# Kernel optimization log

Hardware: AMD Instinct MI355X
Metric: run time of the kernel (lower is better)

## Reference

```python
import jax, jax.numpy as jnp
import numpy as np

SHIFTS = 1
WINDOW_SIZES = (4, 8, 16)
BN_EPS = 1e-5


def _calc_attn_path(x, ws, shifts):
    # x: (b, H, W, 2c) with channels laid out as (qv=2, c)
    b, H, W, c2 = x.shape
    c = c2 // 2
    if shifts > 0:
        x = jnp.roll(x, shift=(-ws // 2, -ws // 2), axis=(1, 2))
    h, w = H // ws, W // ws
    # 'b (h dh) (w dw) (qv c) -> qv (b h w) (dh dw c)'
    qv = x.reshape(b, h, ws, w, ws, 2, c).transpose(5, 0, 1, 3, 2, 4, 6)
    qv = qv.reshape(2, b * h * w, ws * ws * c)
    q, v = qv[0], qv[1]                       # (N, D), N = b*h*w windows, D = ws*ws*c
    atn = jax.nn.softmax(q @ q.T, axis=-1)    # (N, N) attention across windows (as in source)
    y = atn @ v                               # (N, D)
    # '(b h w) (dh dw c) -> b (h dh) (w dw) c'
    y = y.reshape(b, h, w, ws, ws, c).transpose(0, 1, 3, 2, 4, 5).reshape(b, H, W, c)
    if shifts > 0:
        y = jnp.roll(y, shift=(ws // 2, ws // 2), axis=(1, 2))
    return y, atn


def setup_inputs() -> dict:
    key = jax.random.key(0)
    ks = jax.random.split(key, 3)
    B, H, W, C = 4, 128, 128, 180
    inputs = jax.random.normal(ks[0], (B, H, W, C), jnp.float32)
    conv1_w = jax.random.normal(ks[1], (1, 1, C, 2 * C), jnp.float32) * 0.05
    conv1_b = jnp.zeros((2 * C,), jnp.float32)
    bn_scale = jnp.ones((2 * C,), jnp.float32)
    bn_bias = jnp.zeros((2 * C,), jnp.float32)
    conv2_w = jax.random.normal(ks[2], (1, 1, C, C), jnp.float32) * 0.05
    conv2_b = jnp.zeros((C,), jnp.float32)
    return {"inputs": inputs, "conv1_w": conv1_w, "conv1_b": conv1_b,
            "bn_scale": bn_scale, "bn_bias": bn_bias,
            "conv2_w": conv2_w, "conv2_b": conv2_b}


def reference(inputs, conv1_w, conv1_b, bn_scale, bn_bias, conv2_w, conv2_b):
    # 1x1 conv to 2*C channels (calc_attn=True)
    x = jnp.einsum('bhwc,cd->bhwd', inputs, conv1_w[0, 0]) + conv1_b
    # BatchNorm in training mode (batch statistics)
    mean = x.mean(axis=(0, 1, 2))
    var = x.var(axis=(0, 1, 2))
    x = (x - mean) * jax.lax.rsqrt(var + BN_EPS) * bn_scale + bn_bias
    xs = jnp.split(x, 3, axis=-1)             # three groups of 2*C/3 channels
    ys, attns = [], []
    for ws, xi in zip(WINDOW_SIZES, xs):
        y, a = _calc_attn_path(xi, ws, SHIFTS)
        ys.append(y)
        attns.append(a)
    y = jnp.concatenate(ys, axis=-1)          # back to C channels
    y = jnp.einsum('bhwc,cd->bhwd', y, conv2_w[0, 0]) + conv2_b
    return (y, *attns)
```

## Files before the change

kernel.cpp:

```cpp
#include <hip/hip_runtime.h>

typedef unsigned short u16;
typedef __bf16 bf16x8 __attribute__((ext_vector_type(8)));
typedef float f32x4 __attribute__((ext_vector_type(4)));
typedef u16 u16x4 __attribute__((ext_vector_type(4)));
typedef u16 u16x8 __attribute__((ext_vector_type(8)));

__device__ __forceinline__ u16 f2bf(float v) {
    unsigned u = __float_as_uint(v);
    unsigned r = (u + 0x7fffu + ((u >> 16) & 1u)) >> 16;
    return (u16)r;
}
__device__ __forceinline__ float bf2f(u16 u) { return __uint_as_float(((unsigned)u) << 16); }

__device__ __forceinline__ void async_cp16(const u16* g, u16* l) {
    __builtin_amdgcn_global_load_lds((const __attribute__((address_space(1))) unsigned int*)g,
                                     (__attribute__((address_space(3))) unsigned int*)l, 16, 0, 0);
}

__device__ __forceinline__ int xcd_swz(int local, int n) {
    const int q = n >> 3, r = n & 7;
    const int xcd = local & 7, j = local >> 3;
    const int base = xcd < r ? xcd * (q + 1) : r * (q + 1) + (xcd - r) * q;
    return base + j;
}

#define LKSWZ(tid) ((((tid) & 3) ^ (((tid) >> 3) & 3)) << 3)
#define ROSWZ(lane) (((lane) & 15) * 32 + ((((lane) >> 4) ^ (((lane) >> 1) & 3)) << 3))

__global__ __launch_bounds__(256) void gemm_f32(
    const u16* __restrict__ A, const u16* __restrict__ B,
    float* __restrict__ C, const float* __restrict__ bias,
    int K, int ldc, int n_store)
{
    __shared__ char smem[32768];
    u16* As = (u16*)smem;
    u16* Bs = (u16*)(smem + 8192);
    const int tid = threadIdx.x;
    const int lane = tid & 63;
    const int wave = tid >> 6;
    const int wm = wave >> 1, wn = wave & 1;
    const long m0 = (long)blockIdx.y * 128;
    const long n0 = (long)blockIdx.x * 128;

    f32x4 acc[4][4] = {};
    const int lrow = tid >> 2;
    const int lk = LKSWZ(tid);
    const u16* Ag = A + (m0 + lrow) * (long)K + lk;
    const u16* Bg = B + (n0 + lrow) * (long)K + lk;
    u16* Asl = As + tid * 8;
    u16* Bsl = Bs + tid * 8;
    const long K64 = (long)64 * K;
    const int ro = ROSWZ(lane);
    const int nsteps = K >> 5;

    async_cp16(Ag, Asl);
    async_cp16(Ag + K64, Asl + 2048);
    async_cp16(Bg, Bsl);
    async_cp16(Bg + K64, Bsl + 2048);
    __syncthreads();

    int cur = 0;
    for (int s = 0; s < nsteps; s++) {
        if (s + 1 < nsteps) {
            const int kn = (s + 1) << 5;
            u16* An = Asl + ((cur ^ 1) << 13);
            u16* Bn = Bsl + ((cur ^ 1) << 13);
            async_cp16(Ag + kn, An);
            async_cp16(Ag + kn + K64, An + 2048);
            async_cp16(Bg + kn, Bn);
            async_cp16(Bg + kn + K64, Bn + 2048);
        }
        bf16x8 af[4], bg[4];
        const u16* Asc = As + (cur << 13);
        const u16* Bsc = Bs + (cur << 13);
#pragma unroll
        for (int i = 0; i < 4; i++) af[i] = *(const bf16x8*)(Asc + (wm * 64 + i * 16) * 32 + ro);
#pragma unroll
        for (int j = 0; j < 4; j++) bg[j] = *(const bf16x8*)(Bsc + (wn * 64 + j * 16) * 32 + ro);
#pragma unroll
        for (int i = 0; i < 4; i++)
#pragma unroll
            for (int j = 0; j < 4; j++)
                acc[i][j] = __builtin_amdgcn_mfma_f32_16x16x32_bf16(af[i], bg[j], acc[i][j], 0, 0, 0);
        __syncthreads();
        cur ^= 1;
    }

    float bv[4];
#pragma unroll
    for (int j = 0; j < 4; j++) bv[j] = bias[n0 + wn * 64 + j * 16 + (lane & 15)];

    float* Cs = (float*)smem;
    for (int c = 0; c < 4; c++) {
        __syncthreads();
        if (wm == (c >> 1)) {
#pragma unroll
            for (int ii = 0; ii < 2; ii++) {
                const int i = (c & 1) * 2 + ii;
#pragma unroll
                for (int j = 0; j < 4; j++)
#pragma unroll
                    for (int r = 0; r < 4; r++) {
                        const int lr = ii * 16 + ((lane >> 4) << 2) + r;
                        Cs[lr * 128 + wn * 64 + j * 16 + (lane & 15)] = acc[i][j][r] + bv[j];
                    }
            }
        }
        __syncthreads();
        const int lr = tid >> 3;
        const int cg = (tid & 7) * 16;
        const long rowg = m0 + c * 32 + lr;
#pragma unroll
        for (int e = 0; e < 4; e++) {
            const int colg = cg + e * 4;
            if ((int)n0 + colg < n_store)
                *(f32x4*)(C + rowg * (long)ldc + n0 + colg) = *(const f32x4*)(Cs + lr * 128 + colg);
        }
    }
}

__global__ __launch_bounds__(256) void conv1_gemm(
    const float* __restrict__ A, const u16* __restrict__ B,
    u16* __restrict__ C, const float* __restrict__ bias)
{
    __shared__ char smem[16384];
    u16* As = (u16*)smem;
    u16* Bs = (u16*)(smem + 8192);
    const int tid = threadIdx.x;
    const int lane = tid & 63;
    const int wave = tid >> 6;
    const int wm = wave >> 1, wn = wave & 1;
    const long m0 = (long)blockIdx.y * 128;
    const long n0 = (long)blockIdx.x * 128;

    f32x4 acc[4][4] = {};
    const int lrow = tid >> 2;
    const int lk = LKSWZ(tid);
    const float* Ar0 = A + (m0 + lrow) * 180L;
    const float* Ar1 = Ar0 + 64 * 180L;
    const u16* Bg = B + (n0 + lrow) * 192L + lk;
    u16* Asl = As + tid * 8;
    u16* Bsl = Bs + tid * 8;
    const int ro = ROSWZ(lane);

#pragma unroll
    for (int k0 = 0; k0 < 192; k0 += 32) {
        const int gk = k0 + lk;
        u16x8 oa, ob;
        if (gk + 8 <= 180) {
            f32x4 a0 = *(const f32x4*)(Ar0 + gk), a1 = *(const f32x4*)(Ar0 + gk + 4);
            f32x4 b0 = *(const f32x4*)(Ar1 + gk), b1 = *(const f32x4*)(Ar1 + gk + 4);
#pragma unroll
            for (int c = 0; c < 4; c++) {
                oa[c] = f2bf(a0[c]); oa[4 + c] = f2bf(a1[c]);
                ob[c] = f2bf(b0[c]); ob[4 + c] = f2bf(b1[c]);
            }
        } else if (gk < 180) {
            f32x4 a0 = *(const f32x4*)(Ar0 + gk);
            f32x4 b0 = *(const f32x4*)(Ar1 + gk);
#pragma unroll
            for (int c = 0; c < 4; c++) {
                oa[c] = f2bf(a0[c]); oa[4 + c] = 0;
                ob[c] = f2bf(b0[c]); ob[4 + c] = 0;
            }
        } else {
#pragma unroll
            for (int c = 0; c < 8; c++) { oa[c] = 0; ob[c] = 0; }
        }
        *(u16x8*)Asl = oa;
        *(u16x8*)(Asl + 2048) = ob;
        async_cp16(Bg + k0, Bsl);
        async_cp16(Bg + k0 + 64 * 192, Bsl + 2048);
        __syncthreads();
        bf16x8 af[4], bg[4];
#pragma unroll
        for (int i = 0; i < 4; i++) af[i] = *(const bf16x8*)(As + (wm * 64 + i * 16) * 32 + ro);
#pragma unroll
        for (int j = 0; j < 4; j++) bg[j] = *(const bf16x8*)(Bs + (wn * 64 + j * 16) * 32 + ro);
#pragma unroll
        for (int i = 0; i < 4; i++)
#pragma unroll
            for (int j = 0; j < 4; j++)
                acc[i][j] = __builtin_amdgcn_mfma_f32_16x16x32_bf16(af[i], bg[j], acc[i][j], 0, 0, 0);
        __syncthreads();
    }

    float bv[4];
#pragma unroll
    for (int j = 0; j < 4; j++) bv[j] = bias[n0 + wn * 64 + j * 16 + (lane & 15)];

    u16* Cs = (u16*)smem;
    for (int c = 0; c < 2; c++) {
        __syncthreads();
        if (wm == c) {
#pragma unroll
            for (int i = 0; i < 4; i++)
#pragma unroll
                for (int j = 0; j < 4; j++)
#pragma unroll
                    for (int r = 0; r < 4; r++) {
                        const int lr = i * 16 + ((lane >> 4) << 2) + r;
                        Cs[lr * 128 + wn * 64 + j * 16 + (lane & 15)] = f2bf(acc[i][j][r] + bv[j]);
                    }
        }
        __syncthreads();
        const int lr = tid >> 2;
        const int cg = (tid & 3) * 32;
        const long rowg = m0 + c * 64 + lr;
#pragma unroll
        for (int e = 0; e < 4; e++) {
            const int colg = cg + e * 8;
            *(u16x8*)(C + rowg * 384L + n0 + colg) = *(const u16x8*)(Cs + lr * 128 + colg);
        }
    }
}

__global__ __launch_bounds__(256) void qq_all(
    const u16* __restrict__ q0, const u16* __restrict__ q1, const u16* __restrict__ q2,
    float* __restrict__ S0, float* __restrict__ pG1, float* __restrict__ pG2)
{
    __shared__ char smem[32768];
    u16* As = (u16*)smem;
    u16* Bs = (u16*)(smem + 8192);
    const int bid = blockIdx.x;
    int seg, local;
    if (bid < 528) { seg = 0; local = xcd_swz(bid, 528); }
    else if (bid < 816) { seg = 1; local = xcd_swz(bid - 528, 288); }
    else { seg = 2; local = xcd_swz(bid - 816, 180); }
    const int tX = seg == 0 ? 32 : (seg == 1 ? 8 : 2);
    const int TT = (tX * (tX + 1)) >> 1;
    const int K = seg == 0 ? 1024 : (seg == 1 ? 3840 : 15360);
    const int Ksplit = seg == 0 ? 1024 : (seg == 1 ? 480 : 256);
    const int N = seg == 0 ? 4096 : (seg == 1 ? 1024 : 256);
    const u16* A = seg == 0 ? q0 : (seg == 1 ? q1 : q2);
    float* outP = seg == 0 ? S0 : (seg == 1 ? pG1 : pG2);
    const int z = local / TT;
    int rem = local - z * TT;
    int by = 0, rowlen = tX;
    while (rem >= rowlen) { rem -= rowlen; by++; rowlen--; }
    const int bx = by + rem;

    const int tid = threadIdx.x;
    const int lane = tid & 63;
    const int wave = tid >> 6;
    const int wm = wave >> 1, wn = wave & 1;
    const long m0 = (long)by * 128;
    const long n0 = (long)bx * 128;
    const int kbeg = z * Ksplit;

    f32x4 acc[4][4] = {};
    const int lrow = tid >> 2;
    const int lk = LKSWZ(tid);
    const u16* Ag = A + (m0 + lrow) * (long)K + lk;
    const u16* Bg = A + (n0 + lrow) * (long)K + lk;
    u16* Asl = As + tid * 8;
    u16* Bsl = Bs + tid * 8;
    const long K64 = (long)64 * K;
    const int ro = ROSWZ(lane);
    const int nsteps = Ksplit >> 5;

    async_cp16(Ag + kbeg, Asl);
    async_cp16(Ag + kbeg + K64, Asl + 2048);
    async_cp16(Bg + kbeg, Bsl);
    async_cp16(Bg + kbeg + K64, Bsl + 2048);
    __syncthreads();

    int cur = 0;
    for (int s = 0; s < nsteps; s++) {
        if (s + 1 < nsteps) {
            const int kn = kbeg + ((s + 1) << 5);
            u16* An = Asl + ((cur ^ 1) << 13);
            u16* Bn = Bsl + ((cur ^ 1) << 13);
            async_cp16(Ag + kn, An);
            async_cp16(Ag + kn + K64, An + 2048);
            async_cp16(Bg + kn, Bn);
            async_cp16(Bg + kn + K64, Bn + 2048);
        }
        bf16x8 af[4], bg[4];
        const u16* Asc = As + (cur << 13);
        const u16* Bsc = Bs + (cur << 13);
#pragma unroll
        for (int i = 0; i < 4; i++) af[i] = *(const bf16x8*)(Asc + (wm * 64 + i * 16) * 32 + ro);
#pragma unroll
        for (int j = 0; j < 4; j++) bg[j] = *(const bf16x8*)(Bsc + (wn * 64 + j * 16) * 32 + ro);
#pragma unroll
        for (int i = 0; i < 4; i++)
#pragma unroll
            for (int j = 0; j < 4; j++)
                acc[i][j] = __builtin_amdgcn_mfma_f32_16x16x32_bf16(af[i], bg[j], acc[i][j], 0, 0, 0);
        __syncthreads();
        cur ^= 1;
    }

    float* Pz = outP + (long)z * N * N;

    if (bx != by) {
        const int r0 = (int)n0 + wn * 64 + (lane & 15);
        const int c0 = (int)m0 + wm * 64 + ((lane >> 4) << 2);
#pragma unroll
        for (int j = 0; j < 4; j++) {
            float* rp = Pz + (long)(r0 + j * 16) * N + c0;
#pragma unroll
            for (int i = 0; i < 4; i++)
                *(f32x4*)(rp + i * 16) = acc[i][j];
        }
    }

    float* Cs = (float*)smem;
    for (int c = 0; c < 4; c++) {
        __syncthreads();
        if (wm == (c >> 1)) {
#pragma unroll
            for (int ii = 0; ii < 2; ii++) {
                const int i = (c & 1) * 2 + ii;
#pragma unroll
                for (int j = 0; j < 4; j++)
#pragma unroll
                    for (int r = 0; r < 4; r++) {
                        const int lr = ii * 16 + ((lane >> 4) << 2) + r;
                        Cs[lr * 128 + wn * 64 + j * 16 + (lane & 15)] = acc[i][j][r];
                    }
            }
        }
        __syncthreads();
        const int lr = tid >> 3;
        const int cg = (tid & 7) * 16;
        const long rowg = m0 + c * 32 + lr;
#pragma unroll
        for (int e = 0; e < 4; e++) {
            const int colg = cg + e * 4;
            *(f32x4*)(Pz + rowg * (long)N + n0 + colg) = *(const f32x4*)(Cs + lr * 128 + colg);
        }
    }
}

__global__ __launch_bounds__(256, 4) void pv_all(
    const u16* __restrict__ a0, const u16* __restrict__ a1, const u16* __restrict__ a2,
    const u16* __restrict__ vt0, const u16* __restrict__ vt1, const u16* __restrict__ vt2,
    u16* __restrict__ Ysp, float* __restrict__ pP0, float* __restrict__ pP1)
{
    __shared__ char smem[32768];
    u16* As = (u16*)smem;
    u16* Bs = (u16*)(smem + 8192);
    const int bid = blockIdx.x;
    int seg, local, z = 0;
    if (bid < 512) { seg = 0; const int l = xcd_swz(bid, 512); z = l >> 8; local = l & 255; }
    else if (bid < 752) { seg = 1; local = xcd_swz(bid - 512, 240); }
    else { seg = 2; local = xcd_swz(bid - 752, 240); }
    const int tX = seg == 0 ? 8 : (seg == 1 ? 30 : 120);
    const int K = seg == 0 ? 4096 : (seg == 1 ? 1024 : 256);
    const int Ksplit = seg == 0 ? 2048 : K;
    const int D = seg == 0 ? 960 : (seg == 1 ? 3840 : 15360);
    const int l2ws = 2 + seg;
    const int l2wc = 5 - seg;
    const u16* A = seg == 0 ? a0 : (seg == 1 ? a1 : a2);
    const u16* B = seg == 0 ? vt0 : (seg == 1 ? vt1 : vt2);
    const int bx = local % tX;
    const int by = local / tX;

    const int tid = threadIdx.x;
    const int lane = tid & 63;
    const int wave = tid >> 6;
    const int wm = wave >> 1, wn = wave & 1;
    const long m0 = (long)by * 128;
    const long n0 = (long)bx * 128;
    const int kbeg = z * Ksplit;

    f32x4 acc[4][4] = {};
    const int lrow = tid >> 2;
    const int lk = LKSWZ(tid);
    const u16* Ag = A + (m0 + lrow) * (long)K + lk;
    const u16* Bg = B + (n0 + lrow) * (long)K + lk;
    u16* Asl = As + tid * 8;
    u16* Bsl = Bs + tid * 8;
    const long K64 = (long)64 * K;
    const int ro = ROSWZ(lane);
    const int nsteps = Ksplit >> 5;

    async_cp16(Ag + kbeg, Asl);
    async_cp16(Ag + kbeg + K64, Asl + 2048);
    async_cp16(Bg + kbeg, Bsl);
    async_cp16(Bg + kbeg + K64, Bsl + 2048);
    __syncthreads();

    int cur = 0;
    for (int s = 0; s < nsteps; s++) {
        if (s + 1 < nsteps) {
            const int kn = kbeg + ((s + 1) << 5);
            u16* An = Asl + ((cur ^ 1) << 13);
            u16* Bn = Bsl + ((cur ^ 1) << 13);
            async_cp16(Ag + kn, An);
            async_cp16(Ag + kn + K64, An + 2048);
            async_cp16(Bg + kn, Bn);
            async_cp16(Bg + kn + K64, Bn + 2048);
        }
        bf16x8 af[4], bg[4];
        const u16* Asc = As + (cur << 13);
        const u16* Bsc = Bs + (cur << 13);
#pragma unroll
        for (int i = 0; i < 4; i++) af[i] = *(const bf16x8*)(Asc + (wm * 64 + i * 16) * 32 + ro);
#pragma unroll
        for (int j = 0; j < 4; j++) bg[j] = *(const bf16x8*)(Bsc + (wn * 64 + j * 16) * 32 + ro);
#pragma unroll
        for (int i = 0; i < 4; i++)
#pragma unroll
            for (int j = 0; j < 4; j++)
                acc[i][j] = __builtin_amdgcn_mfma_f32_16x16x32_bf16(af[i], bg[j], acc[i][j], 0, 0, 0);
        __syncthreads();
        cur ^= 1;
    }

    if (seg == 0) {
        float* Pz = (z == 0) ? pP0 : pP1;
        float* Cs = (float*)smem;
        for (int c = 0; c < 4; c++) {
            __syncthreads();
            if (wm == (c >> 1)) {
#pragma unroll
                for (int ii = 0; ii < 2; ii++) {
                    const int i = (c & 1) * 2 + ii;
#pragma unroll
                    for (int j = 0; j < 4; j++)
#pragma unroll
                        for (int r = 0; r < 4; r++) {
                            const int lr = ii * 16 + ((lane >> 4) << 2) + r;
                            Cs[lr * 128 + wn * 64 + j * 16 + (lane & 15)] = acc[i][j][r];
                        }
                }
            }
            __syncthreads();
            const int lr = tid >> 3;
            const int cg = (tid & 7) * 16;
            const long rowg = m0 + c * 32 + lr;
#pragma unroll
            for (int e = 0; e < 4; e++) {
                const int colg = cg + e * 4;
                *(f32x4*)(Pz + rowg * 1024L + n0 + colg) = *(const f32x4*)(Cs + lr * 128 + colg);
            }
        }
        return;
    }

    u16* Cs = (u16*)smem;
    const int wcm = (1 << l2wc) - 1;
    const int wsm = (1 << l2ws) - 1;
    const int sh = 1 << (l2ws - 1);
    for (int c = 0; c < 2; c++) {
        __syncthreads();
        if (wm == c) {
#pragma unroll
            for (int i = 0; i < 4; i++)
#pragma unroll
                for (int j = 0; j < 4; j++)
#pragma unroll
                    for (int r = 0; r < 4; r++) {
                        const int lr = i * 16 + ((lane >> 4) << 2) + r;
                        Cs[lr * 128 + wn * 64 + j * 16 + (lane & 15)] = f2bf(acc[i][j][r]);
                    }
        }
        __syncthreads();
        const int lr = tid >> 2;
        const int cgbase = (tid & 3) * 32;
        const int n = (int)m0 + c * 64 + lr;
        const int wi = n & wcm;
        const int hi = (n >> l2wc) & wcm;
        const int bb = n >> (2 * l2wc);
        const int rowb = (hi << l2ws) + sh;
        const int colb = (wi << l2ws) + sh;
        const long bbase = (long)bb * 128 * 128 * 192 + 60 * seg;
#pragma unroll
        for (int e = 0; e < 8; e++) {
            const int colg = cgbase + e * 4;
            const int d = (int)n0 + colg;
            if (d < D) {
                const int cc = d % 60;
                const int pp = d / 60;
                const int dh = pp >> l2ws;
                const int dw = pp & wsm;
                const int row = (rowb + dh) & 127;
                const int col = (colb + dw) & 127;
                *(u16x4*)(Ysp + bbase + ((long)row * 128 + col) * 192 + cc) =
                    *(const u16x4*)(Cs + lr * 128 + colg);
            }
        }
    }
}

__global__ __launch_bounds__(256) void reduce_scatter_g0(
    const float* __restrict__ pP0, const float* __restrict__ pP1, u16* __restrict__ Ysp)
{
    const int n = blockIdx.x;
    const int d = threadIdx.x * 4;
    if (d >= 960) return;
    const long i = (long)n * 1024 + d;
    f32x4 s = *(const f32x4*)(pP0 + i) + *(const f32x4*)(pP1 + i);
    const int cc = d % 60;
    const int pp = d / 60;
    const int dh = pp >> 2;
    const int dw = pp & 3;
    const int wi = n & 31;
    const int hi = (n >> 5) & 31;
    const int b = n >> 10;
    const int row = ((hi << 2) + dh + 2) & 127;
    const int col = ((wi << 2) + dw + 2) & 127;
    u16x4 o;
#pragma unroll
    for (int c = 0; c < 4; c++) o[c] = f2bf(s[c]);
    *(u16x4*)(Ysp + ((long)((b << 7) + row) * 128 + col) * 192 + cc) = o;
}

__global__ __launch_bounds__(256) void zero_pad(u16* __restrict__ Ysp)
{
    const long r = (long)blockIdx.x * 256 + threadIdx.x;
    u16* p = Ysp + r * 192 + 180;
    const u16x4 z = {0, 0, 0, 0};
    *(u16x4*)(p) = z;
    *(u16x4*)(p + 4) = z;
    *(u16x4*)(p + 8) = z;
}

__global__ __launch_bounds__(192) void prep_all(
    const float* __restrict__ W1, const float* __restrict__ W2,
    const float* __restrict__ b1, const float* __restrict__ b2,
    u16* __restrict__ W1t, u16* __restrict__ W2t,
    float* __restrict__ b1p, float* __restrict__ b2p, float* __restrict__ accum)
{
    const int bid = blockIdx.x;
    const int t = threadIdx.x;
    if (bid < 384) {
        W1t[bid * 192 + t] = (bid < 360 && t < 180) ? f2bf(W1[t * 360 + bid]) : (u16)0;
    } else if (bid < 640) {
        const int n = bid - 384;
        W2t[n * 192 + t] = (n < 180 && t < 180) ? f2bf(W2[t * 180 + n]) : (u16)0;
    } else {
#pragma unroll
        for (int j = 0; j < 4; j++) {
            const int i = t + 192 * j;
            if (i < 384) b1p[i] = (i < 360) ? b1[i] : 0.0f;
            else if (i < 640) { const int k = i - 384; b2p[k] = (k < 180) ? b2[k] : 0.0f; }
            if (i < 768) accum[i] = 0.0f;
        }
    }
}

__global__ __launch_bounds__(384) void bn_stats(const u16* __restrict__ x, float* __restrict__ accum)
{
    const int ch = threadIdx.x;
    const long base = (long)blockIdx.x * 256 * 384;
    float s = 0.0f, s2 = 0.0f;
    for (int r = 0; r < 256; r++) {
        const float v = bf2f(x[base + (long)r * 384 + ch]);
        s += v; s2 += v * v;
    }
    atomicAdd(&accum[ch], s);
    atomicAdd(&accum[384 + ch], s2);
}

__global__ __launch_bounds__(256) void gather_all(
    const u16* __restrict__ x, const float* __restrict__ accum,
    const float* __restrict__ bns, const float* __restrict__ bnb,
    u16* __restrict__ q0, u16* __restrict__ q1, u16* __restrict__ q2,
    u16* __restrict__ vt0, u16* __restrict__ vt1, u16* __restrict__ vt2)
{
    __shared__ u16 t[64][65];
    const int bid = blockIdx.x;
    int seg, local;
    if (bid < 1024) { seg = 0; local = bid; }
    else if (bid < 1984) { seg = 1; local = bid - 1024; }
    else { seg = 2; local = bid - 1984; }
    const int tX = seg == 0 ? 16 : (seg == 1 ? 60 : 240);
    const int N = seg == 0 ? 4096 : (seg == 1 ? 1024 : 256);
    const int D = seg == 0 ? 960 : (seg == 1 ? 3840 : 15360);
    const int Dp = seg == 0 ? 1024 : (seg == 1 ? 3840 : 15360);
    const int l2ws = 2 + seg;
    const int l2wc = 5 - seg;
    u16* q = seg == 0 ? q0 : (seg == 1 ? q1 : q2);
    u16* vt = seg == 0 ? vt0 : (seg == 1 ? vt1 : vt2);
    const int bx = local % tX;
    const int by = local / tX;

    const int d0 = bx * 64;
    const int n0 = by * 64;
    const int tc = threadIdx.x & 63;
    const int tr = threadIdx.x >> 6;

    const int d = d0 + tc;
    const int sh = 1 << (l2ws - 1);
    const int cc = d % 60;
    const int pp = d / 60;
    const int dh = pp >> l2ws;
    const int dw = pp & ((1 << l2ws) - 1);
    const int wcm = (1 << l2wc) - 1;
    const int ch = 120 * seg + cc;
    const float m_q = accum[ch] * (1.0f / 65536.0f);
    const float v_q = accum[384 + ch] * (1.0f / 65536.0f) - m_q * m_q;
    const float seq = bns[ch] * rsqrtf(v_q + 1e-5f);
    const float beq = bnb[ch] - m_q * seq;
    const float m_v = accum[ch + 60] * (1.0f / 65536.0f);
    const float v_v = accum[384 + ch + 60] * (1.0f / 65536.0f) - m_v * m_v;
    const float sev = bns[ch + 60] * rsqrtf(v_v + 1e-5f);
    const float bev = bnb[ch + 60] - m_v * sev;
    const bool valid = d < D;

#pragma unroll 4
    for (int i = 0; i < 16; i++) {
        const int n = n0 + i * 4 + tr;
        const int wi = n & wcm;
        const int hi = (n >> l2wc) & wcm;
        const int b = n >> (2 * l2wc);
        const int row = ((hi << l2ws) + dh + sh) & 127;
        const int col = ((wi << l2ws) + dw + sh) & 127;
        const long src = ((long)((b << 7) + row) * 128 + col) * 384 + ch;
        const float xq = bf2f(x[src]);
        const float xv = bf2f(x[src + 60]);
        q[(long)n * Dp + d] = valid ? f2bf(seq * xq + beq) : (u16)0;
        t[tc][i * 4 + tr] = f2bf(sev * xv + bev);
    }
    __syncthreads();
#pragma unroll 4
    for (int i = 0; i < 16; i++) {
        const int dd = i * 4 + tr;
        vt[(long)(d0 + dd) * N + n0 + tc] = t[dd][tc];
    }
}

template <int VPT>
__device__ __forceinline__ void softmax_body(
    const float* __restrict__ P, int nsplit, long MN, int rowi,
    float* __restrict__ S, u16* __restrict__ Sb)
{
    const int N = VPT * 256;
    const long base = (long)rowi * N;
    float v[VPT];
    float mx = -3.0e38f;
#pragma unroll
    for (int i = 0; i < VPT; i++) {
        const long idx = base + i * 256 + threadIdx.x;
        float val = P[idx];
        for (int z = 1; z < nsplit; z++) val += P[(long)z * MN + idx];
        v[i] = val; mx = fmaxf(mx, val);
    }
#pragma unroll
    for (int o = 32; o > 0; o >>= 1) mx = fmaxf(mx, __shfl_down(mx, o, 64));
    __shared__ float redm[4];
    if ((threadIdx.x & 63) == 0) redm[threadIdx.x >> 6] = mx;
    __syncthreads();
    mx = fmaxf(fmaxf(redm[0], redm[1]), fmaxf(redm[2], redm[3]));
    float s = 0.0f;
#pragma unroll
    for (int i = 0; i < VPT; i++) { v[i] = __expf(v[i] - mx); s += v[i]; }
#pragma unroll
    for (int o = 32; o > 0; o >>= 1) s += __shfl_down(s, o, 64);
    __shared__ float reds[4];
    if ((threadIdx.x & 63) == 0) reds[threadIdx.x >> 6] = s;
    __syncthreads();
    s = reds[0] + reds[1] + reds[2] + reds[3];
    const float inv = 1.0f / s;
#pragma unroll
    for (int i = 0; i < VPT; i++) {
        const float r = v[i] * inv;
        const long idx = base + i * 256 + threadIdx.x;
        S[idx] = r;
        Sb[idx] = f2bf(r);
    }
}

__global__ __launch_bounds__(256) void softmax_all(
    float* __restrict__ S0, const float* __restrict__ pG1, const float* __restrict__ pG2,
    float* __restrict__ out1, float* __restrict__ out2,
    u16* __restrict__ ab0, u16* __restrict__ ab1, u16* __restrict__ ab2)
{
    const int r = blockIdx.x;
    if (r < 4096)      softmax_body<16>(S0, 1, 16777216L, r, S0, ab0);
    else if (r < 5120) softmax_body<4>(pG1, 8, 1048576L, r - 4096, out1, ab1);
    else               softmax_body<1>(pG2, 60, 65536L, r - 5120, out2, ab2);
}

extern "C" void kernel_launch(void* const* d_in, const int* in_sizes, int n_in,
                              void* d_out, int out_size, void* d_ws, size_t ws_size,
                              hipStream_t stream)
{
    const float* in_x = (const float*)d_in[0];
    const float* w1  = (const float*)d_in[1];
    const float* b1  = (const float*)d_in[2];
    const float* bns = (const float*)d_in[3];
    const float* bnb = (const float*)d_in[4];
    const float* w2  = (const float*)d_in[5];
    const float* b2  = (const float*)d_in[6];
    float* out = (float*)d_out;

    char* w = (char*)d_ws;
    u16* atnb0 = (u16*)w;
    size_t off = 33554432;
    u16* x = (u16*)(w + off);
    float* pG1 = (float*)(w + off);
    float* pG2 = (float*)(w + off + 33554432);
    u16* Ysp = (u16*)(w + off);
    float* pP1 = (float*)(w + off + 25165824);
    off += 50331648;
    u16* W1t = (u16*)(w + off);  off += 147456;
    u16* W2t = (u16*)(w + off);  off += 98304;
    float* b1p = (float*)(w + off);   off += 4096;
    float* b2p = (float*)(w + off);   off += 4096;
    float* accum = (float*)(w + off); off += 4096;
    u16* q0 = (u16*)(w + off);  off += 8388608;
    u16* q1 = (u16*)(w + off);  off += 7864320;
    u16* q2 = (u16*)(w + off);  off += 7864320;
    u16* vt0 = (u16*)(w + off); off += 8388608;
    u16* vt1 = (u16*)(w + off); off += 7864320;
    u16* vt2 = (u16*)(w + off); off += 7864320;
    u16* atnb1 = (u16*)(w + off); off += 2097152;
    u16* atnb2 = (u16*)(w + off); off += 131072;
    float* pP0 = (float*)q0;

    float* S0 = out + 11796480L;
    float* S1 = out + 28573696L;
    float* S2 = out + 29622272L;

    prep_all<<<641, 192, 0, stream>>>(w1, w2, b1, b2, W1t, W2t, b1p, b2p, accum);
    conv1_gemm<<<dim3(3, 512), 256, 0, stream>>>(in_x, W1t, x, b1p);
    bn_stats<<<256, 384, 0, stream>>>(x, accum);
    gather_all<<<2944, 256, 0, stream>>>(x, accum, bns, bnb, q0, q1, q2, vt0, vt1, vt2);
    qq_all<<<996, 256, 0, stream>>>(q0, q1, q2, S0, pG1, pG2);
    softmax_all<<<5376, 256, 0, stream>>>(S0, pG1, pG2, S1, S2, atnb0, atnb1, atnb2);
    zero_pad<<<256, 256, 0, stream>>>(Ysp);
    pv_all<<<992, 256, 0, stream>>>(atnb0, atnb1, atnb2, vt0, vt1, vt2, Ysp, pP0, pP1);
    reduce_scatter_g0<<<4096, 256, 0, stream>>>(pP0, pP1, Ysp);
    gemm_f32<<<dim3(2, 512), 256, 0, stream>>>(Ysp, W2t, out, b2p, 192, 180, 180);
}
```

Measured before the change: 421.0 us.

## Triple-buffer LDS K-loop with explicit vmcnt waits in qq and pv GEMMs

Measured after the change: 428.2 us. Within noise of the previous version (+1.7%).

```diff
diff --git a/kernel.cpp b/kernel.cpp
--- a/kernel.cpp
+++ b/kernel.cpp
@@ -216,11 +216,57 @@
     }
 }
 
-__global__ __launch_bounds__(256) void qq_all(
+#define KLOOP_3BUF(Asv, Bsv, Aslv, Bslv, AgV, BgV, kbegV, K64V, nstepsV, roV)                 \
+    {                                                                                          \
+        async_cp16(AgV + kbegV, Aslv);                                                         \
+        async_cp16(AgV + kbegV + K64V, Aslv + 2048);                                           \
+        async_cp16(BgV + kbegV, Bslv);                                                         \
+        async_cp16(BgV + kbegV + K64V, Bslv + 2048);                                           \
+        if (nstepsV > 1) {                                                                     \
+            const int kn = kbegV + 32;                                                         \
+            async_cp16(AgV + kn, Aslv + 8192);                                                 \
+            async_cp16(AgV + kn + K64V, Aslv + 8192 + 2048);                                   \
+            async_cp16(BgV + kn, Bslv + 8192);                                                 \
+            async_cp16(BgV + kn + K64V, Bslv + 8192 + 2048);                                   \
+        }                                                                                      \
+        int rb = 0, wb = 2;                                                                    \
+        for (int s = 0; s < nstepsV; s++) {                                                    \
+            if (s + 1 < nstepsV) { asm volatile("s_waitcnt vmcnt(4)" ::: "memory"); }          \
+            else                 { asm volatile("s_waitcnt vmcnt(0)" ::: "memory"); }          \
+            __builtin_amdgcn_sched_barrier(0);                                                 \
+            __builtin_amdgcn_s_barrier();                                                      \
+            __builtin_amdgcn_sched_barrier(0);                                                 \
+            if (s + 2 < nstepsV) {                                                             \
+                const int kn = kbegV + ((s + 2) << 5);                                         \
+                u16* An = Aslv + wb * 8192;                                                    \
+                u16* Bn = Bslv + wb * 8192;                                                    \
+                async_cp16(AgV + kn, An);                                                      \
+                async_cp16(AgV + kn + K64V, An + 2048);                                        \
+                async_cp16(BgV + kn, Bn);                                                      \
+                async_cp16(BgV + kn + K64V, Bn + 2048);                                        \
+            }                                                                                  \
+            bf16x8 af[4], bgf[4];                                                              \
+            const u16* Asc = Asv + rb * 8192;                                                  \
+            const u16* Bsc = Bsv + rb * 8192;                                                  \
+            _Pragma("unroll")                                                                  \
+            for (int i = 0; i < 4; i++) af[i] = *(const bf16x8*)(Asc + (wm * 64 + i * 16) * 32 + roV); \
+            _Pragma("unroll")                                                                  \
+            for (int j = 0; j < 4; j++) bgf[j] = *(const bf16x8*)(Bsc + (wn * 64 + j * 16) * 32 + roV); \
+            _Pragma("unroll")                                                                  \
+            for (int i = 0; i < 4; i++)                                                        \
+                _Pragma("unroll")                                                              \
+                for (int j = 0; j < 4; j++)                                                    \
+                    acc[i][j] = __builtin_amdgcn_mfma_f32_16x16x32_bf16(af[i], bgf[j], acc[i][j], 0, 0, 0); \
+            rb = rb == 2 ? 0 : rb + 1;                                                         \
+            wb = wb == 2 ? 0 : wb + 1;                                                         \
+        }                                                                                      \
+    }
+
+__global__ __launch_bounds__(256, 3) void qq_all(
     const u16* __restrict__ q0, const u16* __restrict__ q1, const u16* __restrict__ q2,
     float* __restrict__ S0, float* __restrict__ pG1, float* __restrict__ pG2)
 {
-    __shared__ char smem[32768];
+    __shared__ char smem[49152];
     u16* As = (u16*)smem;
     u16* Bs = (u16*)(smem + 8192);
     const int bid = blockIdx.x;
@@ -260,38 +306,7 @@
     const int ro = ROSWZ(lane);
     const int nsteps = Ksplit >> 5;
 
-    async_cp16(Ag + kbeg, Asl);
-    async_cp16(Ag + kbeg + K64, Asl + 2048);
-    async_cp16(Bg + kbeg, Bsl);
-    async_cp16(Bg + kbeg + K64, Bsl + 2048);
-    __syncthreads();
-
-    int cur = 0;
-    for (int s = 0; s < nsteps; s++) {
-        if (s + 1 < nsteps) {
-            const int kn = kbeg + ((s + 1) << 5);
-            u16* An = Asl + ((cur ^ 1) << 13);
-            u16* Bn = Bsl + ((cur ^ 1) << 13);
-            async_cp16(Ag + kn, An);
-            async_cp16(Ag + kn + K64, An + 2048);
-            async_cp16(Bg + kn, Bn);
-            async_cp16(Bg + kn + K64, Bn + 2048);
-        }
-        bf16x8 af[4], bg[4];
-        const u16* Asc = As + (cur << 13);
-        const u16* Bsc = Bs + (cur << 13);
-#pragma unroll
-        for (int i = 0; i < 4; i++) af[i] = *(const bf16x8*)(Asc + (wm * 64 + i * 16) * 32 + ro);
-#pragma unroll
-        for (int j = 0; j < 4; j++) bg[j] = *(const bf16x8*)(Bsc + (wn * 64 + j * 16) * 32 + ro);
-#pragma unroll
-        for (int i = 0; i < 4; i++)
-#pragma unroll
-            for (int j = 0; j < 4; j++)
-                acc[i][j] = __builtin_amdgcn_mfma_f32_16x16x32_bf16(af[i], bg[j], acc[i][j], 0, 0, 0);
-        __syncthreads();
-        cur ^= 1;
-    }
+    KLOOP_3BUF(As, Bs, Asl, Bsl, Ag, Bg, kbeg, K64, nsteps, ro);
 
     float* Pz = outP + (long)z * N * N;
 
@@ -335,12 +350,12 @@
     }
 }
 
-__global__ __launch_bounds__(256, 4) void pv_all(
+__global__ __launch_bounds__(256, 3) void pv_all(
     const u16* __restrict__ a0, const u16* __restrict__ a1, const u16* __restrict__ a2,
     const u16* __restrict__ vt0, const u16* __restrict__ vt1, const u16* __restrict__ vt2,
     u16* __restrict__ Ysp, float* __restrict__ pP0, float* __restrict__ pP1)
 {
-    __shared__ char smem[32768];
+    __shared__ char smem[49152];
     u16* As = (u16*)smem;
     u16* Bs = (u16*)(smem + 8192);
     const int bid = blockIdx.x;
@@ -378,38 +393,7 @@
     const int ro = ROSWZ(lane);
     const int nsteps = Ksplit >> 5;
 
-    async_cp16(Ag + kbeg, Asl);
-    async_cp16(Ag + kbeg + K64, Asl + 2048);
-    async_cp16(Bg + kbeg, Bsl);
-    async_cp16(Bg + kbeg + K64, Bsl + 2048);
-    __syncthreads();
-
-    int cur = 0;
-    for (int s = 0; s < nsteps; s++) {
-        if (s + 1 < nsteps) {
-            const int kn = kbeg + ((s + 1) << 5);
-            u16* An = Asl + ((cur ^ 1) << 13);
-            u16* Bn = Bsl + ((cur ^ 1) << 13);
-            async_cp16(Ag + kn, An);
-            async_cp16(Ag + kn + K64, An + 2048);
-            async_cp16(Bg + kn, Bn);
-            async_cp16(Bg + kn + K64, Bn + 2048);
-        }
-        bf16x8 af[4], bg[4];
-        const u16* Asc = As + (cur << 13);
-        const u16* Bsc = Bs + (cur << 13);
-#pragma unroll
-        for (int i = 0; i < 4; i++) af[i] = *(const bf16x8*)(Asc + (wm * 64 + i * 16) * 32 + ro);
-#pragma unroll
-        for (int j = 0; j < 4; j++) bg[j] = *(const bf16x8*)(Bsc + (wn * 64 + j * 16) * 32 + ro);
-#pragma unroll
-        for (int i = 0; i < 4; i++)
-#pragma unroll
-            for (int j = 0; j < 4; j++)
-                acc[i][j] = __builtin_amdgcn_mfma_f32_16x16x32_bf16(af[i], bg[j], acc[i][j], 0, 0, 0);
-        __syncthreads();
-        cur ^= 1;
-    }
+    KLOOP_3BUF(As, Bs, Asl, Bsl, Ag, Bg, kbeg, K64, nsteps, ro);
 
     if (seg == 0) {
         float* Pz = (z == 0) ? pP0 : pP1;
```

## Fuse BN statistics into conv1 GEMM epilogue and zero-pad into softmax

Applied to the files above, without the earlier changes.

After: 418.7 us. About the same (-0.5%).

```diff
diff --git a/kernel.cpp b/kernel.cpp
--- a/kernel.cpp
+++ b/kernel.cpp
@@ -122,7 +122,7 @@
 
 __global__ __launch_bounds__(256) void conv1_gemm(
     const float* __restrict__ A, const u16* __restrict__ B,
-    u16* __restrict__ C, const float* __restrict__ bias)
+    u16* __restrict__ C, const float* __restrict__ bias, float* __restrict__ accum)
 {
     __shared__ char smem[16384];
     u16* As = (u16*)smem;
@@ -189,6 +189,32 @@
     float bv[4];
 #pragma unroll
     for (int j = 0; j < 4; j++) bv[j] = bias[n0 + wn * 64 + j * 16 + (lane & 15)];
+
+    {
+        float bs[4], bs2[4];
+#pragma unroll
+        for (int j = 0; j < 4; j++) {
+            float s = 0.0f, s2 = 0.0f;
+#pragma unroll
+            for (int i = 0; i < 4; i++)
+#pragma unroll
+                for (int r = 0; r < 4; r++) {
+                    const float v = bf2f(f2bf(acc[i][j][r] + bv[j]));
+                    s += v; s2 += v * v;
+                }
+            s += __shfl_xor(s, 16, 64);  s += __shfl_xor(s, 32, 64);
+            s2 += __shfl_xor(s2, 16, 64); s2 += __shfl_xor(s2, 32, 64);
+            bs[j] = s; bs2[j] = s2;
+        }
+        if (lane < 16) {
+#pragma unroll
+            for (int j = 0; j < 4; j++) {
+                const int ch = (int)n0 + wn * 64 + j * 16 + lane;
+                atomicAdd(&accum[ch], bs[j]);
+                atomicAdd(&accum[384 + ch], bs2[j]);
+            }
+        }
+    }
 
     u16* Cs = (u16*)smem;
     for (int c = 0; c < 2; c++) {
@@ -510,16 +536,6 @@
     *(u16x4*)(Ysp + ((long)((b << 7) + row) * 128 + col) * 192 + cc) = o;
 }
 
-__global__ __launch_bounds__(256) void zero_pad(u16* __restrict__ Ysp)
-{
-    const long r = (long)blockIdx.x * 256 + threadIdx.x;
-    u16* p = Ysp + r * 192 + 180;
-    const u16x4 z = {0, 0, 0, 0};
-    *(u16x4*)(p) = z;
-    *(u16x4*)(p + 4) = z;
-    *(u16x4*)(p + 8) = z;
-}
-
 __global__ __launch_bounds__(192) void prep_all(
     const float* __restrict__ W1, const float* __restrict__ W2,
     const float* __restrict__ b1, const float* __restrict__ b2,
@@ -542,19 +558,6 @@
             if (i < 768) accum[i] = 0.0f;
         }
     }
-}
-
-__global__ __launch_bounds__(384) void bn_stats(const u16* __restrict__ x, float* __restrict__ accum)
-{
-    const int ch = threadIdx.x;
-    const long base = (long)blockIdx.x * 256 * 384;
-    float s = 0.0f, s2 = 0.0f;
-    for (int r = 0; r < 256; r++) {
-        const float v = bf2f(x[base + (long)r * 384 + ch]);
-        s += v; s2 += v * v;
-    }
-    atomicAdd(&accum[ch], s);
-    atomicAdd(&accum[384 + ch], s2);
 }
 
 __global__ __launch_bounds__(256) void gather_all(
@@ -669,9 +672,19 @@
 __global__ __launch_bounds__(256) void softmax_all(
     float* __restrict__ S0, const float* __restrict__ pG1, const float* __restrict__ pG2,
     float* __restrict__ out1, float* __restrict__ out2,
-    u16* __restrict__ ab0, u16* __restrict__ ab1, u16* __restrict__ ab2)
+    u16* __restrict__ ab0, u16* __restrict__ ab1, u16* __restrict__ ab2,
+    u16* __restrict__ Ysp)
 {
     const int r = blockIdx.x;
+    if (r >= 5376) {
+        const long rr = (long)(r - 5376) * 256 + threadIdx.x;
+        u16* p = Ysp + rr * 192 + 180;
+        const u16x4 zz = {0, 0, 0, 0};
+        *(u16x4*)(p) = zz;
+        *(u16x4*)(p + 4) = zz;
+        *(u16x4*)(p + 8) = zz;
+        return;
+    }
     if (r < 4096)      softmax_body<16>(S0, 1, 16777216L, r, S0, ab0);
     else if (r < 5120) softmax_body<4>(pG1, 8, 1048576L, r - 4096, out1, ab1);
     else               softmax_body<1>(pG2, 60, 65536L, r - 5120, out2, ab2);
@@ -719,12 +732,10 @@
     float* S2 = out + 29622272L;
 
     prep_all<<<641, 192, 0, stream>>>(w1, w2, b1, b2, W1t, W2t, b1p, b2p, accum);
-    conv1_gemm<<<dim3(3, 512), 256, 0, stream>>>(in_x, W1t, x, b1p);
-    bn_stats<<<256, 384, 0, stream>>>(x, accum);
+    conv1_gemm<<<dim3(3, 512), 256, 0, stream>>>(in_x, W1t, x, b1p, accum);
     gather_all<<<2944, 256, 0, stream>>>(x, accum, bns, bnb, q0, q1, q2, vt0, vt1, vt2);
     qq_all<<<996, 256, 0, stream>>>(q0, q1, q2, S0, pG1, pG2);
-    softmax_all<<<5376, 256, 0, stream>>>(S0, pG1, pG2, S1, S2, atnb0, atnb1, atnb2);
-    zero_pad<<<256, 256, 0, stream>>>(Ysp);
+    softmax_all<<<5632, 256, 0, stream>>>(S0, pG1, pG2, S1, S2, atnb0, atnb1, atnb2, Ysp);
     pv_all<<<992, 256, 0, stream>>>(atnb0, atnb1, atnb2, vt0, vt1, vt2, Ysp, pP0, pP1);
     reduce_scatter_g0<<<4096, 256, 0, stream>>>(pP0, pP1, Ysp);
     gemm_f32<<<dim3(2, 512), 256, 0, stream>>>(Ysp, W2t, out, b2p, 192, 180, 180);
```
